# Performance work log

Measured on AMD Instinct MI355X. Metric: run time of the kernel, lower is better.

Reference implementation:

```python
import jax, jax.numpy as jnp
import numpy as np

N_NODES = 50000
N_EDGES = 800000
IN_FEATS = 128
H_FEATS = 128
NUM_CLASSES = 64


def _linear_params(key, fan_in, fan_out):
    kw, kb = jax.random.split(key)
    bound = 1.0 / np.sqrt(fan_in)
    W = jax.random.uniform(kw, (fan_out, fan_in), minval=-bound, maxval=bound, dtype=jnp.float32)
    b = jax.random.uniform(kb, (fan_out,), minval=-bound, maxval=bound, dtype=jnp.float32)
    return W, b


def setup_inputs() -> dict:
    key = jax.random.key(0)
    k_feat, k_src, k_dst, k1, k2, k3 = jax.random.split(key, 6)
    in_feat = jax.random.normal(k_feat, (N_NODES, IN_FEATS), dtype=jnp.float32)
    src = jax.random.randint(k_src, (N_EDGES,), 0, N_NODES, dtype=jnp.int32)
    dst = jax.random.randint(k_dst, (N_EDGES,), 0, N_NODES, dtype=jnp.int32)
    W1, b1 = _linear_params(k1, IN_FEATS, H_FEATS)
    W2, b2 = _linear_params(k2, H_FEATS, H_FEATS)
    W3, b3 = _linear_params(k3, H_FEATS, NUM_CLASSES)
    return {"in_feat": in_feat, "W1": W1, "b1": b1, "W2": W2, "b2": b2,
            "W3": W3, "b3": b3, "src": src, "dst": dst}


def reference(in_feat, W1, b1, W2, b2, W3, b3, src, dst):
    N = in_feat.shape[0]

    def gin_layer(x, W, b):
        # DGL GINConv with eps=0: (x + sum of in-neighbor messages) -> Linear
        agg = jax.ops.segment_sum(x[src], dst, num_segments=N)  # [N, d]
        return jax.nn.relu((x + agg) @ W.T + b)

    h = gin_layer(in_feat, W1, b1)
    h = gin_layer(h, W2, b2)
    h = gin_layer(h, W3, b3)
    return h
```

## Files before the change

kernel.cpp:

```cpp
#include <hip/hip_runtime.h>

typedef _Float16 half8 __attribute__((ext_vector_type(8)));
typedef _Float16 half2v __attribute__((ext_vector_type(2)));
typedef float floatx4 __attribute__((ext_vector_type(4)));
typedef unsigned int uintx4 __attribute__((ext_vector_type(4)));

union AB { uint4 u; half8 h; };
union H2 { unsigned int u; _Float16 h[2]; };
union H2P { unsigned int u; half2v h; };
union US16 { uintx4 u[2]; unsigned short s[16]; };

#define CAPLOG 6
#define CAP 64

__global__ __launch_bounds__(256) void histA_init_k(
    const int* __restrict__ dst, int* __restrict__ histG, int E, int nbins,
    const float* __restrict__ W1, const float* __restrict__ W2, const float* __restrict__ W3,
    _Float16* __restrict__ W1h, _Float16* __restrict__ W2h, _Float16* __restrict__ W3h,
    _Float16* __restrict__ z1, _Float16* __restrict__ h1, _Float16* __restrict__ hZ,
    int n4w1, int n4w2, int n4w3, int zoff128, int zoff64) {
    int t = threadIdx.x;
    if (blockIdx.x < 256) {
        __shared__ int h[256];
        h[t] = 0;
        __syncthreads();
        int per = (E + 255) / 256;
        int beg = blockIdx.x * per;
        int end = min(E, beg + per);
        for (int e = beg + t; e < end; e += 256)
            atomicAdd(&h[dst[e] >> 8], 1);
        __syncthreads();
        for (int i = t; i < nbins; i += 256)
            histG[i * 256 + blockIdx.x] = h[i];
        return;
    }
    int i = (blockIdx.x - 256) * 256 + t;
    const float* X;
    _Float16* O;
    int j;
    if (i < n4w1) { X = W1; O = W1h; j = i; }
    else if (i < n4w1 + n4w2) { X = W2; O = W2h; j = i - n4w1; }
    else if (i < n4w1 + n4w2 + n4w3) { X = W3; O = W3h; j = i - n4w1 - n4w2; }
    else {
        int z = i - (n4w1 + n4w2 + n4w3);
        if (z < 16) ((uint4*)z1)[zoff128 + z] = make_uint4(0, 0, 0, 0);
        else if (z < 32) ((uint4*)h1)[zoff128 + (z - 16)] = make_uint4(0, 0, 0, 0);
        else if (z < 40) ((uint4*)hZ)[zoff64 + (z - 32)] = make_uint4(0, 0, 0, 0);
        return;
    }
    float4 v = reinterpret_cast<const float4*>(X)[j];
    union { uint2 u; _Float16 h[4]; } o;
    o.h[0] = (_Float16)v.x; o.h[1] = (_Float16)v.y;
    o.h[2] = (_Float16)v.z; o.h[3] = (_Float16)v.w;
    reinterpret_cast<uint2*>(O)[j] = o.u;
}

__global__ __launch_bounds__(1024) void scan1_k(const int* __restrict__ x,
                                                int* __restrict__ inc,
                                                int* __restrict__ partial, int n) {
    __shared__ int sd[1024];
    int t = threadIdx.x;
    int v = blockIdx.x * 1024 + t;
    sd[t] = (v < n) ? x[v] : 0;
    __syncthreads();
    for (int off = 1; off < 1024; off <<= 1) {
        int val = (t >= off) ? sd[t - off] : 0;
        __syncthreads();
        sd[t] += val;
        __syncthreads();
    }
    if (v < n) inc[v] = sd[t];
    if (t == 1023) partial[blockIdx.x] = sd[1023];
}

__global__ __launch_bounds__(256) void scatterB_k(const int* __restrict__ src,
                                                  const int* __restrict__ dst,
                                                  const int* __restrict__ inc,
                                                  const int* __restrict__ histG,
                                                  const int* __restrict__ partial, int nparts,
                                                  unsigned int* __restrict__ binned,
                                                  int E, int nbins) {
    __shared__ int cur[256];
    __shared__ int pp[64];
    int t = threadIdx.x, blk = blockIdx.x;
    if (t < 64) {
        int v = (t < nparts) ? partial[t] : 0;
        for (int off = 1; off < 64; off <<= 1) {
            int n = __shfl_up(v, off, 64);
            if (t >= off) v += n;
        }
        int ex = __shfl_up(v, 1, 64);
        if (t == 0) ex = 0;
        pp[t] = ex;
    }
    __syncthreads();
    for (int i = t; i < nbins; i += 256) {
        int idx = i * 256 + blk;
        cur[i] = inc[idx] + pp[idx >> 10] - histG[idx];
    }
    __syncthreads();
    int per = (E + 255) / 256;
    int beg = blk * per;
    int end = min(E, beg + per);
    for (int e = beg + t; e < end; e += 256) {
        int d = dst[e];
        int s = src[e];
        int pos = atomicAdd(&cur[d >> 8], 1);
        binned[pos] = ((unsigned int)(d & 255) << 16) | (unsigned int)s;
    }
}

__global__ __launch_bounds__(256) void binB_k(const unsigned int* __restrict__ binned,
                                              const int* __restrict__ inc,
                                              const int* __restrict__ histG,
                                              const int* __restrict__ partial, int nparts,
                                              unsigned short* __restrict__ col,
                                              int* __restrict__ cnt,
                                              int N, int E, int nbins) {
    __shared__ unsigned short lcol[256 * CAP];
    __shared__ int lcnt[256];
    __shared__ int pp[64];
    __shared__ int bounds[2];
    int t = threadIdx.x;
    int b = blockIdx.x;
    if (t < 64) {
        int v = (t < nparts) ? partial[t] : 0;
        for (int off = 1; off < 64; off <<= 1) {
            int n = __shfl_up(v, off, 64);
            if (t >= off) v += n;
        }
        int ex = __shfl_up(v, 1, 64);
        if (t == 0) ex = 0;
        pp[t] = ex;
    }
    unsigned int* lcol32 = (unsigned int*)lcol;
    for (int i = t; i < 256 * CAP / 2; i += 256) lcol32[i] = 0xFFFFFFFFu;
    lcnt[t] = 0;
    __syncthreads();
    if (t == 0) {
        int i0 = b * 256;
        bounds[0] = inc[i0] + pp[i0 >> 10] - histG[i0];
    } else if (t == 1) {
        if (b == nbins - 1) bounds[1] = E;
        else {
            int i1 = (b + 1) * 256;
            bounds[1] = inc[i1] + pp[i1 >> 10] - histG[i1];
        }
    }
    __syncthreads();
    int beg = bounds[0], end = bounds[1];
    for (int e = beg + t; e < end; e += 256) {
        unsigned int u = binned[e];
        int dl = u >> 16;
        int pos = atomicAdd(&lcnt[dl], 1);
        if (pos < CAP) lcol[(dl << CAPLOG) + pos] = (unsigned short)(u & 0xFFFFu);
    }
    __syncthreads();
    int base = b << 8;
    int nodes = min(256, N - base);
    uint4* colg = (uint4*)(col + ((size_t)base << CAPLOG));
    const uint4* coll = (const uint4*)lcol;
    for (int i = t; i < nodes * 8; i += 256) colg[i] = coll[i];
    for (int i = t; i < nodes; i += 256) cnt[base + i] = lcnt[i];
}

__global__ __launch_bounds__(256) void gemm_z1_k(const float* __restrict__ X,
                                                 const _Float16* __restrict__ Wh,
                                                 _Float16* __restrict__ z1, int nnodes) {
    constexpr int WSTR = 136;
    __shared__ _Float16 Wl[128 * WSTR];

    const int t = threadIdx.x;
    for (int p = t; p < 128 * 16; p += 256) {
        int f = p >> 4;
        int kq = (p & 15) * 8;
        *reinterpret_cast<uint4*>(&Wl[f * WSTR + kq]) =
            *reinterpret_cast<const uint4*>(Wh + f * 128 + kq);
    }
    __syncthreads();

    const int wave = t >> 6;
    const int lane = t & 63;
    const int quad = lane >> 4;
    const int fcol = lane & 15;
    const int m_base = (blockIdx.x * 4 + wave) * 16;
    const int row = m_base + fcol;
    const bool rowok = row < nnodes;

    floatx4 acc[8];
#pragma unroll
    for (int ft = 0; ft < 8; ft++) acc[ft] = (floatx4){0.f, 0.f, 0.f, 0.f};

    const float* Xrow = X + (size_t)row * 128;
#pragma unroll
    for (int step = 0; step < 4; step++) {
        AB a;
        if (rowok) {
            float4 f0 = *reinterpret_cast<const float4*>(Xrow + step * 32 + quad * 8);
            float4 f1 = *reinterpret_cast<const float4*>(Xrow + step * 32 + quad * 8 + 4);
            a.h[0] = (_Float16)f0.x; a.h[1] = (_Float16)f0.y;
            a.h[2] = (_Float16)f0.z; a.h[3] = (_Float16)f0.w;
            a.h[4] = (_Float16)f1.x; a.h[5] = (_Float16)f1.y;
            a.h[6] = (_Float16)f1.z; a.h[7] = (_Float16)f1.w;
        } else a.u = make_uint4(0u, 0u, 0u, 0u);
#pragma unroll
        for (int ft = 0; ft < 8; ft++) {
            half8 b = *reinterpret_cast<const half8*>(
                &Wl[(ft * 16 + fcol) * WSTR + step * 32 + quad * 8]);
            acc[ft] = __builtin_amdgcn_mfma_f32_16x16x32_f16(a.h, b, acc[ft], 0, 0, 0);
        }
    }

#pragma unroll
    for (int ft = 0; ft < 8; ft++) {
        int f = ft * 16 + fcol;
#pragma unroll
        for (int r = 0; r < 4; r++) {
            int node = m_base + quad * 4 + r;
            if (node < nnodes)
                z1[(size_t)node * 128 + f] = (_Float16)acc[ft][r];
        }
    }
}

__global__ __launch_bounds__(256) void agg_z1_k(const _Float16* __restrict__ Z,
                                                const int* __restrict__ cnt,
                                                const unsigned short* __restrict__ col,
                                                const float* __restrict__ bias,
                                                _Float16* __restrict__ H, int nnodes) {
    int w = blockIdx.x * 4 + (threadIdx.x >> 6);
    int lane = threadIdx.x & 63;
    if (w >= nnodes) return;
    const unsigned int* Z32 = reinterpret_cast<const unsigned int*>(Z);
    int deg = cnt[w];
    if (deg > CAP) deg = CAP;
    int degp = (deg + 15) & ~15;
    const unsigned short* c = col + ((size_t)w << CAPLOG);

    H2P acc[16];
#pragma unroll
    for (int j = 0; j < 16; j++) acc[j].u = 0u;

    for (int e = 0; e < degp; e += 16) {
        US16 ix;
        ix.u[0] = *reinterpret_cast<const uintx4*>(c + e);
        ix.u[1] = *reinterpret_cast<const uintx4*>(c + e + 8);
        H2P u[16];
#pragma unroll
        for (int j = 0; j < 16; j++) {
            int s = (int)ix.s[j];
            s = (s < nnodes) ? s : nnodes;
            u[j].u = Z32[(size_t)s * 64 + lane];
        }
#pragma unroll
        for (int j = 0; j < 16; j++) acc[j].h += u[j].h;
    }

    float s0 = 0.f, s1 = 0.f;
#pragma unroll
    for (int j = 0; j < 16; j++) {
        s0 += (float)acc[j].h[0];
        s1 += (float)acc[j].h[1];
    }
    float2 bv = reinterpret_cast<const float2*>(bias)[lane];
    H2 xs, r;
    xs.u = Z32[(size_t)w * 64 + lane];
    r.h[0] = (_Float16)fmaxf((float)xs.h[0] + s0 + bv.x, 0.f);
    r.h[1] = (_Float16)fmaxf((float)xs.h[1] + s1 + bv.y, 0.f);
    __builtin_nontemporal_store(r.u, reinterpret_cast<unsigned int*>(H) + (size_t)w * 64 + lane);
}

__global__ __launch_bounds__(256) void aggregate_k(const _Float16* __restrict__ X,
                                                   const int* __restrict__ cnt,
                                                   const unsigned short* __restrict__ col,
                                                   _Float16* __restrict__ Y,
                                                   int nnodes) {
    int w = blockIdx.x * 4 + (threadIdx.x >> 6);
    int lane = threadIdx.x & 63;
    if (w >= nnodes) return;
    const unsigned int* X32 = reinterpret_cast<const unsigned int*>(X);
    int deg = cnt[w];
    if (deg > CAP) deg = CAP;
    int degp = (deg + 15) & ~15;
    const unsigned short* c = col + ((size_t)w << CAPLOG);

    H2P acc[16];
#pragma unroll
    for (int j = 0; j < 16; j++) acc[j].u = 0u;

    for (int e = 0; e < degp; e += 16) {
        US16 ix;
        ix.u[0] = *reinterpret_cast<const uintx4*>(c + e);
        ix.u[1] = *reinterpret_cast<const uintx4*>(c + e + 8);
        H2P u[16];
#pragma unroll
        for (int j = 0; j < 16; j++) {
            int s = (int)ix.s[j];
            s = (s < nnodes) ? s : nnodes;
            u[j].u = X32[(size_t)s * 64 + lane];
        }
#pragma unroll
        for (int j = 0; j < 16; j++) acc[j].h += u[j].h;
    }

    float s0 = 0.f, s1 = 0.f;
#pragma unroll
    for (int j = 0; j < 16; j++) {
        s0 += (float)acc[j].h[0];
        s1 += (float)acc[j].h[1];
    }
    H2 xs, r;
    xs.u = X32[(size_t)w * 64 + lane];
    r.h[0] = (_Float16)((float)xs.h[0] + s0);
    r.h[1] = (_Float16)((float)xs.h[1] + s1);
    __builtin_nontemporal_store(r.u, reinterpret_cast<unsigned int*>(Y) + (size_t)w * 64 + lane);
}

__global__ __launch_bounds__(256) void agg_final_k(const _Float16* __restrict__ Z,
                                                   const int* __restrict__ cnt,
                                                   const unsigned short* __restrict__ col,
                                                   const float* __restrict__ bias,
                                                   float* __restrict__ out, int nnodes) {
    int lane = threadIdx.x & 63;
    int fl = lane & 31;
    int node = blockIdx.x * 8 + (threadIdx.x >> 6) * 2 + (lane >> 5);
    if (node >= nnodes) return;
    const unsigned int* Z32 = (const unsigned int*)Z;

    int deg = cnt[node];
    if (deg > CAP) deg = CAP;
    int degp = (deg + 15) & ~15;
    const unsigned short* c = col + ((size_t)node << CAPLOG);

    H2P acc[16];
#pragma unroll
    for (int j = 0; j < 16; j++) acc[j].u = 0u;

    for (int e = 0; e < degp; e += 16) {
        US16 ix;
        ix.u[0] = *reinterpret_cast<const uintx4*>(c + e);
        ix.u[1] = *reinterpret_cast<const uintx4*>(c + e + 8);
        H2P u[16];
#pragma unroll
        for (int j = 0; j < 16; j++) {
            int s = (int)ix.s[j];
            s = (s < nnodes) ? s : nnodes;
            u[j].u = Z32[(size_t)s * 32 + fl];
        }
#pragma unroll
        for (int j = 0; j < 16; j++) acc[j].h += u[j].h;
    }

    float s0 = 0.f, s1 = 0.f;
#pragma unroll
    for (int j = 0; j < 16; j++) {
        s0 += (float)acc[j].h[0];
        s1 += (float)acc[j].h[1];
    }
    H2 xs;
    xs.u = Z32[(size_t)node * 32 + fl];
    float2 bv = reinterpret_cast<const float2*>(bias)[fl];
    float2 r;
    r.x = fmaxf((float)xs.h[0] + s0 + bv.x, 0.f);
    r.y = fmaxf((float)xs.h[1] + s1 + bv.y, 0.f);
    reinterpret_cast<float2*>(out)[(size_t)node * 32 + fl] = r;
}

__global__ __launch_bounds__(256) void gemm23_k(const _Float16* __restrict__ Y,
                                                const _Float16* __restrict__ W2h,
                                                const float* __restrict__ b2,
                                                const _Float16* __restrict__ W3h,
                                                _Float16* __restrict__ hZ, int nnodes) {
    constexpr int WSTR = 136;
    __shared__ _Float16 Wl[128 * WSTR];
    __shared__ _Float16 Hl[64 * WSTR];
    __shared__ float Bl[128];

    const int t = threadIdx.x;
    for (int p = t; p < 128 * 16; p += 256) {
        int f = p >> 4;
        int kq = (p & 15) * 8;
        *reinterpret_cast<uint4*>(&Wl[f * WSTR + kq]) =
            *reinterpret_cast<const uint4*>(W2h + f * 128 + kq);
    }
    if (t < 128) Bl[t] = b2[t];
    __syncthreads();

    const int wave = t >> 6;
    const int lane = t & 63;
    const int quad = lane >> 4;
    const int fcol = lane & 15;
    const int m_base = (blockIdx.x * 4 + wave) * 16;
    const int row = m_base + fcol;
    const bool rowok = row < nnodes;

    floatx4 acc[8];
#pragma unroll
    for (int ft = 0; ft < 8; ft++) acc[ft] = (floatx4){0.f, 0.f, 0.f, 0.f};

    const uint4* Yrow = reinterpret_cast<const uint4*>(Y + (size_t)row * 128);
#pragma unroll
    for (int step = 0; step < 4; step++) {
        AB a;
        if (rowok) a.u = Yrow[step * 4 + quad];
        else       a.u = make_uint4(0u, 0u, 0u, 0u);
#pragma unroll
        for (int ft = 0; ft < 8; ft++) {
            half8 b = *reinterpret_cast<const half8*>(
                &Wl[(ft * 16 + fcol) * WSTR + step * 32 + quad * 8]);
            acc[ft] = __builtin_amdgcn_mfma_f32_16x16x32_f16(a.h, b, acc[ft], 0, 0, 0);
        }
    }

#pragma unroll
    for (int ft = 0; ft < 8; ft++) {
        int f = ft * 16 + fcol;
        float bv = Bl[f];
#pragma unroll
        for (int r = 0; r < 4; r++) {
            int nl = wave * 16 + quad * 4 + r;
            Hl[nl * WSTR + f] = (_Float16)fmaxf(acc[ft][r] + bv, 0.f);
        }
    }
    __syncthreads();

    for (int p = t; p < 64 * 16; p += 256) {
        int f = p >> 4;
        int kq = (p & 15) * 8;
        *reinterpret_cast<uint4*>(&Wl[f * WSTR + kq]) =
            *reinterpret_cast<const uint4*>(W3h + f * 128 + kq);
    }
    __syncthreads();

    floatx4 acc2[4];
#pragma unroll
    for (int ft = 0; ft < 4; ft++) acc2[ft] = (floatx4){0.f, 0.f, 0.f, 0.f};
#pragma unroll
    for (int step = 0; step < 4; step++) {
        AB a;
        a.h = *reinterpret_cast<const half8*>(
            &Hl[(wave * 16 + fcol) * WSTR + step * 32 + quad * 8]);
#pragma unroll
        for (int ft = 0; ft < 4; ft++) {
            half8 b = *reinterpret_cast<const half8*>(
                &Wl[(ft * 16 + fcol) * WSTR + step * 32 + quad * 8]);
            acc2[ft] = __builtin_amdgcn_mfma_f32_16x16x32_f16(a.h, b, acc2[ft], 0, 0, 0);
        }
    }
#pragma unroll
    for (int ft = 0; ft < 4; ft++) {
        int f = ft * 16 + fcol;
#pragma unroll
        for (int r = 0; r < 4; r++) {
            int node = m_base + quad * 4 + r;
            if (node < nnodes)
                hZ[(size_t)node * 64 + f] = (_Float16)acc2[ft][r];
        }
    }
}

extern "C" void kernel_launch(void* const* d_in, const int* in_sizes, int n_in,
                              void* d_out, int out_size, void* d_ws, size_t ws_size,
                              hipStream_t stream) {
    const float* in_feat = (const float*)d_in[0];
    const float* W1 = (const float*)d_in[1];
    const float* b1 = (const float*)d_in[2];
    const float* W2 = (const float*)d_in[3];
    const float* b2 = (const float*)d_in[4];
    const float* W3 = (const float*)d_in[5];
    const float* b3 = (const float*)d_in[6];
    const int* src = (const int*)d_in[7];
    const int* dst = (const int*)d_in[8];
    float* out = (float*)d_out;

    const int N = in_sizes[0] / 128;
    const int E = in_sizes[7];
    const int szW1 = in_sizes[1];
    const int szW2 = in_sizes[3];
    const int szW3 = in_sizes[5];
    const int nbins = (N + 255) >> 8;
    const int nhist = nbins * 256;

    char* p = (char*)d_ws;
    int* cnt = (int*)p;               p += (size_t)N * 4;
    unsigned short* col = (unsigned short*)p; p += (size_t)N * CAP * 2;
    int* histG = (int*)p;             p += (size_t)nhist * 4;
    int* incS = (int*)p;              p += (size_t)nhist * 4;
    int* partial = (int*)p;           p += 256;
    unsigned int* binned = (unsigned int*)p; p += (size_t)E * 4;
    _Float16* z1 = (_Float16*)p;      p += (size_t)(N + 1) * 128 * 2;
    _Float16* h1 = (_Float16*)p;      p += (size_t)(N + 1) * 128 * 2;
    _Float16* hB = (_Float16*)p;      p += (size_t)N * 128 * 2;
    _Float16* hZ = (_Float16*)p;      p += (size_t)(N + 1) * 64 * 2;
    _Float16* W1h = (_Float16*)p;     p += (size_t)szW1 * 2;
    _Float16* W2h = (_Float16*)p;     p += (size_t)szW2 * 2;
    _Float16* W3h = (_Float16*)p;     p += (size_t)szW3 * 2;

    const int nblk_scan = (nhist + 1023) / 1024;

    {
        int total = szW1 / 4 + szW2 / 4 + szW3 / 4 + 40;
        int iblk = (total + 255) / 256;
        histA_init_k<<<256 + iblk, 256, 0, stream>>>(dst, histG, E, nbins,
                                                     W1, W2, W3, W1h, W2h, W3h,
                                                     z1, h1, hZ,
                                                     szW1 / 4, szW2 / 4, szW3 / 4,
                                                     N * 16, N * 8);
    }
    scan1_k<<<nblk_scan, 1024, 0, stream>>>(histG, incS, partial, nhist);
    scatterB_k<<<256, 256, 0, stream>>>(src, dst, incS, histG, partial, nblk_scan,
                                        binned, E, nbins);
    binB_k<<<nbins, 256, 0, stream>>>(binned, incS, histG, partial, nblk_scan,
                                      col, cnt, N, E, nbins);

    const int nblk_agg = (N + 3) / 4;
    const int nblk_gemm = (N + 63) / 64;
    gemm_z1_k<<<nblk_gemm, 256, 0, stream>>>(in_feat, W1h, z1, N);
    agg_z1_k<<<nblk_agg, 256, 0, stream>>>(z1, cnt, col, b1, h1, N);
    aggregate_k<<<nblk_agg, 256, 0, stream>>>(h1, cnt, col, hB, N);
    gemm23_k<<<nblk_gemm, 256, 0, stream>>>(hB, W2h, b2, W3h, hZ, N);
    agg_final_k<<<(N + 7) / 8, 256, 0, stream>>>(hZ, cnt, col, b3, out, N);
}
```

Before: 222.4 us.

## Interleave CSR column slots and gather 16-byte rows across edge-parallel lane groups

```diff
diff --git a/kernel.cpp b/kernel.cpp
--- a/kernel.cpp
+++ b/kernel.cpp
@@ -8,7 +8,6 @@
 union AB { uint4 u; half8 h; };
 union H2 { unsigned int u; _Float16 h[2]; };
 union H2P { unsigned int u; half2v h; };
-union US16 { uintx4 u[2]; unsigned short s[16]; };
 
 #define CAPLOG 6
 #define CAP 64
@@ -153,7 +152,8 @@
         unsigned int u = binned[e];
         int dl = u >> 16;
         int pos = atomicAdd(&lcnt[dl], 1);
-        if (pos < CAP) lcol[(dl << CAPLOG) + pos] = (unsigned short)(u & 0xFFFFu);
+        if (pos < CAP)
+            lcol[(dl << CAPLOG) + ((pos & 3) << 4) + (pos >> 2)] = (unsigned short)(u & 0xFFFFu);
     }
     __syncthreads();
     int base = b << 8;
@@ -223,7 +223,7 @@
     }
 }
 
-__global__ __launch_bounds__(256) void agg_z1_k(const _Float16* __restrict__ Z,
+__global__ __launch_bounds__(256) void agg128_k(const _Float16* __restrict__ Z,
                                                 const int* __restrict__ cnt,
                                                 const unsigned short* __restrict__ col,
                                                 const float* __restrict__ bias,
@@ -231,89 +231,83 @@
     int w = blockIdx.x * 4 + (threadIdx.x >> 6);
     int lane = threadIdx.x & 63;
     if (w >= nnodes) return;
-    const unsigned int* Z32 = reinterpret_cast<const unsigned int*>(Z);
+    const int q = lane >> 4;
+    const int c15 = lane & 15;
+    const unsigned int* X32 = reinterpret_cast<const unsigned int*>(Z);
     int deg = cnt[w];
     if (deg > CAP) deg = CAP;
-    int degp = (deg + 15) & ~15;
-    const unsigned short* c = col + ((size_t)w << CAPLOG);
-
-    H2P acc[16];
-#pragma unroll
-    for (int j = 0; j < 16; j++) acc[j].u = 0u;
-
-    for (int e = 0; e < degp; e += 16) {
-        US16 ix;
-        ix.u[0] = *reinterpret_cast<const uintx4*>(c + e);
-        ix.u[1] = *reinterpret_cast<const uintx4*>(c + e + 8);
-        H2P u[16];
-#pragma unroll
-        for (int j = 0; j < 16; j++) {
-            int s = (int)ix.s[j];
-            s = (s < nnodes) ? s : nnodes;
-            u[j].u = Z32[(size_t)s * 64 + lane];
-        }
-#pragma unroll
-        for (int j = 0; j < 16; j++) acc[j].h += u[j].h;
-    }
-
-    float s0 = 0.f, s1 = 0.f;
-#pragma unroll
-    for (int j = 0; j < 16; j++) {
-        s0 += (float)acc[j].h[0];
-        s1 += (float)acc[j].h[1];
-    }
-    float2 bv = reinterpret_cast<const float2*>(bias)[lane];
-    H2 xs, r;
-    xs.u = Z32[(size_t)w * 64 + lane];
-    r.h[0] = (_Float16)fmaxf((float)xs.h[0] + s0 + bv.x, 0.f);
-    r.h[1] = (_Float16)fmaxf((float)xs.h[1] + s1 + bv.y, 0.f);
-    __builtin_nontemporal_store(r.u, reinterpret_cast<unsigned int*>(H) + (size_t)w * 64 + lane);
-}
-
-__global__ __launch_bounds__(256) void aggregate_k(const _Float16* __restrict__ X,
-                                                   const int* __restrict__ cnt,
-                                                   const unsigned short* __restrict__ col,
-                                                   _Float16* __restrict__ Y,
-                                                   int nnodes) {
-    int w = blockIdx.x * 4 + (threadIdx.x >> 6);
-    int lane = threadIdx.x & 63;
-    if (w >= nnodes) return;
-    const unsigned int* X32 = reinterpret_cast<const unsigned int*>(X);
-    int deg = cnt[w];
-    if (deg > CAP) deg = CAP;
-    int degp = (deg + 15) & ~15;
-    const unsigned short* c = col + ((size_t)w << CAPLOG);
-
-    H2P acc[16];
-#pragma unroll
-    for (int j = 0; j < 16; j++) acc[j].u = 0u;
-
-    for (int e = 0; e < degp; e += 16) {
-        US16 ix;
-        ix.u[0] = *reinterpret_cast<const uintx4*>(c + e);
-        ix.u[1] = *reinterpret_cast<const uintx4*>(c + e + 8);
-        H2P u[16];
-#pragma unroll
-        for (int j = 0; j < 16; j++) {
-            int s = (int)ix.s[j];
-            s = (s < nnodes) ? s : nnodes;
-            u[j].u = X32[(size_t)s * 64 + lane];
-        }
-#pragma unroll
-        for (int j = 0; j < 16; j++) acc[j].h += u[j].h;
-    }
-
-    float s0 = 0.f, s1 = 0.f;
-#pragma unroll
-    for (int j = 0; j < 16; j++) {
-        s0 += (float)acc[j].h[0];
-        s1 += (float)acc[j].h[1];
-    }
-    H2 xs, r;
-    xs.u = X32[(size_t)w * 64 + lane];
-    r.h[0] = (_Float16)((float)xs.h[0] + s0);
-    r.h[1] = (_Float16)((float)xs.h[1] + s1);
-    __builtin_nontemporal_store(r.u, reinterpret_cast<unsigned int*>(Y) + (size_t)w * 64 + lane);
+    int nb = (deg + 15) >> 4;
+    const unsigned short* c = col + ((size_t)w << CAPLOG) + (q << 4);
+
+    H2P a0[4], a1[4], a2[4], a3[4];
+#pragma unroll
+    for (int m = 0; m < 4; m++) { a0[m].u = 0u; a1[m].u = 0u; a2[m].u = 0u; a3[m].u = 0u; }
+
+    for (int t = 0; t < nb; t++) {
+        uint2 iw = *reinterpret_cast<const uint2*>(c + t * 4);
+        int s0 = (int)(iw.x & 0xFFFFu); s0 = (s0 < nnodes) ? s0 : nnodes;
+        int s1 = (int)(iw.x >> 16);     s1 = (s1 < nnodes) ? s1 : nnodes;
+        int s2 = (int)(iw.y & 0xFFFFu); s2 = (s2 < nnodes) ? s2 : nnodes;
+        int s3 = (int)(iw.y >> 16);     s3 = (s3 < nnodes) ? s3 : nnodes;
+        uint4 v0 = *reinterpret_cast<const uint4*>(X32 + (size_t)s0 * 64 + c15 * 4);
+        uint4 v1 = *reinterpret_cast<const uint4*>(X32 + (size_t)s1 * 64 + c15 * 4);
+        uint4 v2 = *reinterpret_cast<const uint4*>(X32 + (size_t)s2 * 64 + c15 * 4);
+        uint4 v3 = *reinterpret_cast<const uint4*>(X32 + (size_t)s3 * 64 + c15 * 4);
+        H2P u;
+        u.u = v0.x; a0[0].h += u.h;  u.u = v0.y; a0[1].h += u.h;
+        u.u = v0.z; a0[2].h += u.h;  u.u = v0.w; a0[3].h += u.h;
+        u.u = v1.x; a1[0].h += u.h;  u.u = v1.y; a1[1].h += u.h;
+        u.u = v1.z; a1[2].h += u.h;  u.u = v1.w; a1[3].h += u.h;
+        u.u = v2.x; a2[0].h += u.h;  u.u = v2.y; a2[1].h += u.h;
+        u.u = v2.z; a2[2].h += u.h;  u.u = v2.w; a2[3].h += u.h;
+        u.u = v3.x; a3[0].h += u.h;  u.u = v3.y; a3[1].h += u.h;
+        u.u = v3.z; a3[2].h += u.h;  u.u = v3.w; a3[3].h += u.h;
+    }
+#pragma unroll
+    for (int m = 0; m < 4; m++) {
+        a0[m].h += a1[m].h;
+        a2[m].h += a3[m].h;
+        a0[m].h += a2[m].h;
+    }
+    float fs[8];
+#pragma unroll
+    for (int m = 0; m < 4; m++) {
+        fs[2 * m] = (float)a0[m].h[0];
+        fs[2 * m + 1] = (float)a0[m].h[1];
+    }
+#pragma unroll
+    for (int m = 0; m < 8; m++) fs[m] += __shfl_xor(fs[m], 16, 64);
+#pragma unroll
+    for (int m = 0; m < 8; m++) fs[m] += __shfl_xor(fs[m], 32, 64);
+
+    if (q == 0) {
+        uint4 sv = *reinterpret_cast<const uint4*>(X32 + (size_t)w * 64 + c15 * 4);
+        H2 x0, x1, x2, x3;
+        x0.u = sv.x; x1.u = sv.y; x2.u = sv.z; x3.u = sv.w;
+        float o[8];
+        o[0] = (float)x0.h[0] + fs[0]; o[1] = (float)x0.h[1] + fs[1];
+        o[2] = (float)x1.h[0] + fs[2]; o[3] = (float)x1.h[1] + fs[3];
+        o[4] = (float)x2.h[0] + fs[4]; o[5] = (float)x2.h[1] + fs[5];
+        o[6] = (float)x3.h[0] + fs[6]; o[7] = (float)x3.h[1] + fs[7];
+        if (bias) {
+            float4 b0 = *reinterpret_cast<const float4*>(bias + c15 * 8);
+            float4 b1 = *reinterpret_cast<const float4*>(bias + c15 * 8 + 4);
+            o[0] = fmaxf(o[0] + b0.x, 0.f); o[1] = fmaxf(o[1] + b0.y, 0.f);
+            o[2] = fmaxf(o[2] + b0.z, 0.f); o[3] = fmaxf(o[3] + b0.w, 0.f);
+            o[4] = fmaxf(o[4] + b1.x, 0.f); o[5] = fmaxf(o[5] + b1.y, 0.f);
+            o[6] = fmaxf(o[6] + b1.z, 0.f); o[7] = fmaxf(o[7] + b1.w, 0.f);
+        }
+        H2 r0, r1, r2, r3;
+        r0.h[0] = (_Float16)o[0]; r0.h[1] = (_Float16)o[1];
+        r1.h[0] = (_Float16)o[2]; r1.h[1] = (_Float16)o[3];
+        r2.h[0] = (_Float16)o[4]; r2.h[1] = (_Float16)o[5];
+        r3.h[0] = (_Float16)o[6]; r3.h[1] = (_Float16)o[7];
+        uintx4 ov;
+        ov.x = r0.u; ov.y = r1.u; ov.z = r2.u; ov.w = r3.u;
+        __builtin_nontemporal_store(
+            ov, reinterpret_cast<uintx4*>(reinterpret_cast<unsigned int*>(H) +
+                                          (size_t)w * 64 + c15 * 4));
+    }
 }
 
 __global__ __launch_bounds__(256) void agg_final_k(const _Float16* __restrict__ Z,
@@ -322,48 +316,76 @@
                                                    const float* __restrict__ bias,
                                                    float* __restrict__ out, int nnodes) {
     int lane = threadIdx.x & 63;
-    int fl = lane & 31;
+    int sub = lane & 31;
     int node = blockIdx.x * 8 + (threadIdx.x >> 6) * 2 + (lane >> 5);
     if (node >= nnodes) return;
+    const int q = sub >> 3;
+    const int c7 = sub & 7;
     const unsigned int* Z32 = (const unsigned int*)Z;
-
     int deg = cnt[node];
     if (deg > CAP) deg = CAP;
-    int degp = (deg + 15) & ~15;
-    const unsigned short* c = col + ((size_t)node << CAPLOG);
-
-    H2P acc[16];
-#pragma unroll
-    for (int j = 0; j < 16; j++) acc[j].u = 0u;
-
-    for (int e = 0; e < degp; e += 16) {
-        US16 ix;
-        ix.u[0] = *reinterpret_cast<const uintx4*>(c + e);
-        ix.u[1] = *reinterpret_cast<const uintx4*>(c + e + 8);
-        H2P u[16];
-#pragma unroll
-        for (int j = 0; j < 16; j++) {
-            int s = (int)ix.s[j];
-            s = (s < nnodes) ? s : nnodes;
-            u[j].u = Z32[(size_t)s * 32 + fl];
-        }
-#pragma unroll
-        for (int j = 0; j < 16; j++) acc[j].h += u[j].h;
-    }
-
-    float s0 = 0.f, s1 = 0.f;
-#pragma unroll
-    for (int j = 0; j < 16; j++) {
-        s0 += (float)acc[j].h[0];
-        s1 += (float)acc[j].h[1];
-    }
-    H2 xs;
-    xs.u = Z32[(size_t)node * 32 + fl];
-    float2 bv = reinterpret_cast<const float2*>(bias)[fl];
-    float2 r;
-    r.x = fmaxf((float)xs.h[0] + s0 + bv.x, 0.f);
-    r.y = fmaxf((float)xs.h[1] + s1 + bv.y, 0.f);
-    reinterpret_cast<float2*>(out)[(size_t)node * 32 + fl] = r;
+    int nb = (deg + 15) >> 4;
+    const unsigned short* c = col + ((size_t)node << CAPLOG) + (q << 4);
+
+    H2P a0[4], a1[4], a2[4], a3[4];
+#pragma unroll
+    for (int m = 0; m < 4; m++) { a0[m].u = 0u; a1[m].u = 0u; a2[m].u = 0u; a3[m].u = 0u; }
+
+    for (int t = 0; t < nb; t++) {
+        uint2 iw = *reinterpret_cast<const uint2*>(c + t * 4);
+        int s0 = (int)(iw.x & 0xFFFFu); s0 = (s0 < nnodes) ? s0 : nnodes;
+        int s1 = (int)(iw.x >> 16);     s1 = (s1 < nnodes) ? s1 : nnodes;
+        int s2 = (int)(iw.y & 0xFFFFu); s2 = (s2 < nnodes) ? s2 : nnodes;
+        int s3 = (int)(iw.y >> 16);     s3 = (s3 < nnodes) ? s3 : nnodes;
+        uint4 v0 = *reinterpret_cast<const uint4*>(Z32 + (size_t)s0 * 32 + c7 * 4);
+        uint4 v1 = *reinterpret_cast<const uint4*>(Z32 + (size_t)s1 * 32 + c7 * 4);
+        uint4 v2 = *reinterpret_cast<const uint4*>(Z32 + (size_t)s2 * 32 + c7 * 4);
+        uint4 v3 = *reinterpret_cast<const uint4*>(Z32 + (size_t)s3 * 32 + c7 * 4);
+        H2P u;
+        u.u = v0.x; a0[0].h += u.h;  u.u = v0.y; a0[1].h += u.h;
+        u.u = v0.z; a0[2].h += u.h;  u.u = v0.w; a0[3].h += u.h;
+        u.u = v1.x; a1[0].h += u.h;  u.u = v1.y; a1[1].h += u.h;
+        u.u = v1.z; a1[2].h += u.h;  u.u = v1.w; a1[3].h += u.h;
+        u.u = v2.x; a2[0].h += u.h;  u.u = v2.y; a2[1].h += u.h;
+        u.u = v2.z; a2[2].h += u.h;  u.u = v2.w; a2[3].h += u.h;
+        u.u = v3.x; a3[0].h += u.h;  u.u = v3.y; a3[1].h += u.h;
+        u.u = v3.z; a3[2].h += u.h;  u.u = v3.w; a3[3].h += u.h;
+    }
+#pragma unroll
+    for (int m = 0; m < 4; m++) {
+        a0[m].h += a1[m].h;
+        a2[m].h += a3[m].h;
+        a0[m].h += a2[m].h;
+    }
+    float fs[8];
+#pragma unroll
+    for (int m = 0; m < 4; m++) {
+        fs[2 * m] = (float)a0[m].h[0];
+        fs[2 * m + 1] = (float)a0[m].h[1];
+    }
+#pragma unroll
+    for (int m = 0; m < 8; m++) fs[m] += __shfl_xor(fs[m], 8, 64);
+#pragma unroll
+    for (int m = 0; m < 8; m++) fs[m] += __shfl_xor(fs[m], 16, 64);
+
+    if (q == 0) {
+        uint4 sv = *reinterpret_cast<const uint4*>(Z32 + (size_t)node * 32 + c7 * 4);
+        H2 x0, x1, x2, x3;
+        x0.u = sv.x; x1.u = sv.y; x2.u = sv.z; x3.u = sv.w;
+        float4 b0 = *reinterpret_cast<const float4*>(bias + c7 * 8);
+        float4 b1 = *reinterpret_cast<const float4*>(bias + c7 * 8 + 4);
+        float4 w0, w1;
+        w0.x = fmaxf((float)x0.h[0] + fs[0] + b0.x, 0.f);
+        w0.y = fmaxf((float)x0.h[1] + fs[1] + b0.y, 0.f);
+        w0.z = fmaxf((float)x1.h[0] + fs[2] + b0.z, 0.f);
+        w0.w = fmaxf((float)x1.h[1] + fs[3] + b0.w, 0.f);
+        w1.x = fmaxf((float)x2.h[0] + fs[4] + b1.x, 0.f);
+        w1.y = fmaxf((float)x2.h[1] + fs[5] + b1.y, 0.f);
+        w1.z = fmaxf((float)x3.h[0] + fs[6] + b1.z, 0.f);
+        w1.w = fmaxf((float)x3.h[1] + fs[7] + b1.w, 0.f);
+        *reinterpret_cast<float4*>(out + (size_t)node * 64 + c7 * 8) = w0;
+        *reinterpret_cast<float4*>(out + (size_t)node * 64 + c7 * 8 + 4) = w1;
+    }
 }
 
 __global__ __launch_bounds__(256) void gemm23_k(const _Float16* __restrict__ Y,
@@ -516,8 +538,8 @@
     const int nblk_agg = (N + 3) / 4;
     const int nblk_gemm = (N + 63) / 64;
     gemm_z1_k<<<nblk_gemm, 256, 0, stream>>>(in_feat, W1h, z1, N);
-    agg_z1_k<<<nblk_agg, 256, 0, stream>>>(z1, cnt, col, b1, h1, N);
-    aggregate_k<<<nblk_agg, 256, 0, stream>>>(h1, cnt, col, hB, N);
+    agg128_k<<<nblk_agg, 256, 0, stream>>>(z1, cnt, col, b1, h1, N);
+    agg128_k<<<nblk_agg, 256, 0, stream>>>(h1, cnt, col, nullptr, hB, N);
     gemm23_k<<<nblk_gemm, 256, 0, stream>>>(hB, W2h, b2, W3h, hZ, N);
     agg_final_k<<<(N + 7) / 8, 256, 0, stream>>>(hZ, cnt, col, b3, out, N);
 }
```

Result: no change. 223.1 us (+0.3%).
